# Kernel optimization log

Hardware: AMD Instinct MI355X
Metric: run time of the kernel (lower is better)

The kernel has to match this reference:

```python
import jax, jax.numpy as jnp
import numpy as np

T, B, IN, H, OUT = 2048, 64, 32, 512, 32


def setup_inputs() -> dict:
    key = jax.random.key(0)
    ks = jax.random.split(key, 7)
    s = 1.0 / np.sqrt(H)
    return {
        "inputs": jax.random.normal(ks[0], (T, B, IN), dtype=jnp.float32),
        "h0": jnp.zeros((B, H), dtype=jnp.float32),
        "c0": jnp.zeros((B, H), dtype=jnp.float32),
        "W_ih": jax.random.uniform(ks[1], (4 * H, IN), minval=-s, maxval=s, dtype=jnp.float32),
        "W_hh": jax.random.uniform(ks[2], (4 * H, H), minval=-s, maxval=s, dtype=jnp.float32),
        "b_ih": jax.random.uniform(ks[3], (4 * H,), minval=-s, maxval=s, dtype=jnp.float32),
        "b_hh": jax.random.uniform(ks[4], (4 * H,), minval=-s, maxval=s, dtype=jnp.float32),
        "W_out": jax.random.uniform(ks[5], (OUT, H), minval=-s, maxval=s, dtype=jnp.float32),
        "b_out": jax.random.uniform(ks[6], (OUT,), minval=-s, maxval=s, dtype=jnp.float32),
    }


def reference(inputs, h0, c0, W_ih, W_hh, b_ih, b_hh, W_out, b_out):
    Hh = h0.shape[-1]
    # Precompute input projections for all timesteps: [T, B, 4H]
    x_proj = jnp.einsum('tbi,gi->tbg', inputs, W_ih) + b_ih + b_hh

    def step(carry, xp):
        h, c = carry
        gates = xp + h @ W_hh.T  # [B, 4H]
        i, f, g, o = jnp.split(gates, 4, axis=-1)  # torch LSTMCell gate order
        i = jax.nn.sigmoid(i)
        f = jax.nn.sigmoid(f)
        g = jnp.tanh(g)
        o = jax.nn.sigmoid(o)
        c_new = f * c + i * g
        h_new = o * jnp.tanh(c_new)
        return (h_new, c_new), h_new

    (h_T, c_T), h_all = jax.lax.scan(step, (h0, c0), x_proj)
    outputs = jnp.einsum('tbh,oh->tbo', h_all, W_out) + b_out  # [T, B, OUT]
    return outputs, (h_T, c_T)
```

## Files before the change

kernel.cpp:

```cpp
#include <hip/hip_runtime.h>

#define TT 2048
#define BB 64
#define INF 32
#define HH 512
#define OO 32

typedef __attribute__((ext_vector_type(8))) short bf16x8;
typedef __attribute__((ext_vector_type(4))) float f32x4;

__device__ __forceinline__ float sigm(float x) {
  return 1.f / (1.f + __expf(-x));
}
__device__ __forceinline__ float tanh_(float x) {
  float e = __expf(2.f * x);
  return 1.f - 2.f / (1.f + e);
}
__device__ __forceinline__ unsigned short f2bf(float f) {
  unsigned u = __float_as_uint(f);
  u = (u + 0x7FFFu + ((u >> 16) & 1u)) >> 16;
  return (unsigned short)u;
}
__device__ __forceinline__ float bf2f(unsigned short s) {
  return __uint_as_float(((unsigned)s) << 16);
}

#define COH_LOAD4(dst, ptr)                                                  \
  asm volatile("global_load_dwordx4 %0, %1, off sc0 sc1"                     \
               : "=v"(dst) : "v"(ptr))

#define SPIN_LIMIT 20000

#define HSTR 528

__global__ __launch_bounds__(512, 2)
void lstm_fused(const float* __restrict__ X,
                const float* __restrict__ h0,
                const float* __restrict__ c0,
                const float* __restrict__ Wih,
                const float* __restrict__ Whh,
                const float* __restrict__ bih,
                const float* __restrict__ bhh,
                const float* __restrict__ Wout,
                const float* __restrict__ bout,
                float* __restrict__ outp,
                float* __restrict__ hT,
                float* __restrict__ cT,
                unsigned short* __restrict__ hring,
                int* __restrict__ flags)
{
  const int tid    = threadIdx.x;
  const int rg     = tid >> 6;
  const int lane   = tid & 63;
  const int bg     = blockIdx.x & 7;
  const int sl     = blockIdx.x >> 3;
  const int bglob0 = bg << 3;

  __shared__ __align__(16) unsigned short hlds[8 * HSTR];

  const bool mwave = (rg < 4);

  bf16x8 aW[16], aX;
  float biasf[4];
  if (mwave) {
    const int ri = lane & 15;
    const int arow = ((ri & 3) << 9) + (sl << 4) + (rg << 2) + (ri >> 2);
    const float* wb = Whh + (size_t)arow * HH + ((lane >> 4) << 3);
#pragma unroll
    for (int kt = 0; kt < 16; ++kt) {
      float4 a = ((const float4*)(wb + kt * 32))[0];
      float4 b = ((const float4*)(wb + kt * 32))[1];
      bf16x8 f;
      f[0] = (short)f2bf(a.x); f[1] = (short)f2bf(a.y);
      f[2] = (short)f2bf(a.z); f[3] = (short)f2bf(a.w);
      f[4] = (short)f2bf(b.x); f[5] = (short)f2bf(b.y);
      f[6] = (short)f2bf(b.z); f[7] = (short)f2bf(b.w);
      aW[kt] = f;
    }
    const float* wi = Wih + (size_t)arow * INF + ((lane >> 4) << 3);
    float4 a = ((const float4*)wi)[0];
    float4 b = ((const float4*)wi)[1];
    aX[0] = (short)f2bf(a.x); aX[1] = (short)f2bf(a.y);
    aX[2] = (short)f2bf(a.z); aX[3] = (short)f2bf(a.w);
    aX[4] = (short)f2bf(b.x); aX[5] = (short)f2bf(b.y);
    aX[6] = (short)f2bf(b.z); aX[7] = (short)f2bf(b.w);
#pragma unroll
    for (int r = 0; r < 4; ++r) {
      int grow = (r << 9) + (sl << 4) + (rg << 2) + (lane >> 4);
      biasf[r] = bih[grow] + bhh[grow];
    }
  }
  float wout[8];
  {
    const float4* wp = (const float4*)(Wout + sl * HH + (lane << 3));
    float4 a = wp[0], b4 = wp[1];
    wout[0] = a.x;  wout[1] = a.y;  wout[2] = a.z;  wout[3] = a.w;
    wout[4] = b4.x; wout[5] = b4.y; wout[6] = b4.z; wout[7] = b4.w;
  }
  const float bo = bout[sl];

  const bool owner = mwave && ((lane & 15) < 8);
  const int ob = lane & 7;
  const int ojj = (rg << 2) + (lane >> 4);
  const int hoff_owner = (bglob0 + ob) * HH + (sl << 4) + ojj;
  float cst = owner ? c0[hoff_owner] : 0.f;

  const int lb = tid >> 6, lg = tid & 63;
  int* myflags = flags + (bg << 5);

  for (int t = 0; t < TT; ++t) {
    bf16x8 bx;
    if (mwave) {
      const float* xr = X + (size_t)t * BB * INF + (bglob0 + (lane & 7)) * INF
                        + ((lane >> 4) << 3);
      float4 xva = ((const float4*)xr)[0];
      float4 xvb = ((const float4*)xr)[1];
      bx[0] = (short)f2bf(xva.x); bx[1] = (short)f2bf(xva.y);
      bx[2] = (short)f2bf(xva.z); bx[3] = (short)f2bf(xva.w);
      bx[4] = (short)f2bf(xvb.x); bx[5] = (short)f2bf(xvb.y);
      bx[6] = (short)f2bf(xvb.z); bx[7] = (short)f2bf(xvb.w);
    }

    if (t > 0) {
      int f = __hip_atomic_load(&myflags[lane & 31], __ATOMIC_RELAXED,
                                __HIP_MEMORY_SCOPE_AGENT);
      int guard = 0;
      while (__any(f < t)) {
        if (++guard > SPIN_LIMIT) break;
        __builtin_amdgcn_s_sleep(1);
        f = __hip_atomic_load(&myflags[lane & 31], __ATOMIC_RELAXED,
                              __HIP_MEMORY_SCOPE_AGENT);
      }
    }

    if (t == 0) {
      const float* hp = h0 + (size_t)(bglob0 + lb) * HH + (lg << 3);
      float4 a = ((const float4*)hp)[0];
      float4 b = ((const float4*)hp)[1];
      unsigned d0 = (unsigned)f2bf(a.x) | ((unsigned)f2bf(a.y) << 16);
      unsigned d1 = (unsigned)f2bf(a.z) | ((unsigned)f2bf(a.w) << 16);
      unsigned d2 = (unsigned)f2bf(b.x) | ((unsigned)f2bf(b.y) << 16);
      unsigned d3 = (unsigned)f2bf(b.z) | ((unsigned)f2bf(b.w) << 16);
      *(int4*)(hlds + lb * HSTR + (lg << 3)) = make_int4(d0, d1, d2, d3);
    } else {
      const unsigned short* hsrc = hring + (size_t)((t - 1) & 1) * BB * HH
                                   + (size_t)(bglob0 + lb) * HH + (lg << 3);
      int4 hv;
      COH_LOAD4(hv, hsrc);
      asm volatile("s_waitcnt vmcnt(0)" ::: "memory");
      __builtin_amdgcn_sched_barrier(0);
      *(int4*)(hlds + lb * HSTR + (lg << 3)) = hv;
    }
    __syncthreads();

    float o0 = 0.f, o1 = 0.f;
    if (mwave) {
      f32x4 acc0 = {0.f, 0.f, 0.f, 0.f};
      f32x4 acc1 = {0.f, 0.f, 0.f, 0.f};
      acc0 = __builtin_amdgcn_mfma_f32_16x16x32_bf16(aX, bx, acc0, 0, 0, 0);
      const unsigned short* hb = hlds + (lane & 7) * HSTR + ((lane >> 4) << 3);
#pragma unroll
      for (int kt = 0; kt < 16; kt += 2) {
        bf16x8 bf0 = *(const bf16x8*)(hb + kt * 32);
        bf16x8 bf1 = *(const bf16x8*)(hb + (kt + 1) * 32);
        acc0 = __builtin_amdgcn_mfma_f32_16x16x32_bf16(aW[kt], bf0, acc0, 0, 0, 0);
        acc1 = __builtin_amdgcn_mfma_f32_16x16x32_bf16(aW[kt + 1], bf1, acc1, 0, 0, 0);
      }
      float i_ = sigm(acc0[0] + acc1[0] + biasf[0]);
      float f_ = sigm(acc0[1] + acc1[1] + biasf[1]);
      float g_ = tanh_(acc0[2] + acc1[2] + biasf[2]);
      float o_ = sigm(acc0[3] + acc1[3] + biasf[3]);
      float cnew = __fmaf_rn(f_, cst, i_ * g_);
      float hv = o_ * tanh_(cnew);
      if (owner) cst = cnew;
      float hv2 = __shfl(hv, (lane + 16) & 63, 64);
      if (owner && ((lane >> 4) & 1) == 0) {
        unsigned pk = (unsigned)f2bf(hv) | ((unsigned)f2bf(hv2) << 16);
        unsigned* slot32 = (unsigned*)(hring + (size_t)(t & 1) * BB * HH);
        __hip_atomic_store(
            &slot32[((bglob0 + ob) << 8) + (sl << 3) + (rg << 1) + (lane >> 5)],
            pk, __ATOMIC_RELAXED, __HIP_MEMORY_SCOPE_AGENT);
      }
      if (owner && t == TT - 1) { hT[hoff_owner] = hv; cT[hoff_owner] = cst; }
    } else {
      const int wb2 = (rg - 4) << 1;
      const bf16x8 ha = *(const bf16x8*)(hlds + wb2 * HSTR + (lane << 3));
      const bf16x8 hc = *(const bf16x8*)(hlds + (wb2 + 1) * HSTR + (lane << 3));
#pragma unroll
      for (int j = 0; j < 8; ++j) {
        o0 = __fmaf_rn(bf2f((unsigned short)ha[j]), wout[j], o0);
        o1 = __fmaf_rn(bf2f((unsigned short)hc[j]), wout[j], o1);
      }
#pragma unroll
      for (int s = 32; s >= 1; s >>= 1) {
        o0 += __shfl_xor(o0, s, 64);
        o1 += __shfl_xor(o1, s, 64);
      }
    }
    __syncthreads();
    if (tid == 0)
      __hip_atomic_store(&myflags[sl], t + 1, __ATOMIC_RELAXED,
                         __HIP_MEMORY_SCOPE_AGENT);
    if (!mwave && t > 0 && lane == 0) {
      const int wb2 = (rg - 4) << 1;
      outp[(size_t)(t - 1) * BB * OO + (bglob0 + wb2) * OO + sl] = o0 + bo;
      outp[(size_t)(t - 1) * BB * OO + (bglob0 + wb2 + 1) * OO + sl] = o1 + bo;
    }
  }

  {
    int f = __hip_atomic_load(&myflags[lane & 31], __ATOMIC_RELAXED,
                              __HIP_MEMORY_SCOPE_AGENT);
    int guard = 0;
    while (__any(f < TT)) {
      if (++guard > SPIN_LIMIT) break;
      __builtin_amdgcn_s_sleep(1);
      f = __hip_atomic_load(&myflags[lane & 31], __ATOMIC_RELAXED,
                            __HIP_MEMORY_SCOPE_AGENT);
    }
  }
  {
    const unsigned short* hb = hring + (size_t)((TT - 1) & 1) * BB * HH
                               + (size_t)(bglob0 + rg) * HH + (lane << 3);
    int4 p;
    COH_LOAD4(p, hb);
    asm volatile("s_waitcnt vmcnt(0)" ::: "memory");
    __builtin_amdgcn_sched_barrier(0);
    float oacc =
        __uint_as_float(((unsigned)p.x) << 16)        * wout[0] +
        __uint_as_float(((unsigned)p.x) & 0xFFFF0000u) * wout[1] +
        __uint_as_float(((unsigned)p.y) << 16)        * wout[2] +
        __uint_as_float(((unsigned)p.y) & 0xFFFF0000u) * wout[3] +
        __uint_as_float(((unsigned)p.z) << 16)        * wout[4] +
        __uint_as_float(((unsigned)p.z) & 0xFFFF0000u) * wout[5] +
        __uint_as_float(((unsigned)p.w) << 16)        * wout[6] +
        __uint_as_float(((unsigned)p.w) & 0xFFFF0000u) * wout[7];
#pragma unroll
    for (int s = 32; s >= 1; s >>= 1) oacc += __shfl_xor(oacc, s, 64);
    if (lane == 0)
      outp[(size_t)(TT - 1) * BB * OO + (bglob0 + rg) * OO + sl] = oacc + bo;
  }
}

extern "C" void kernel_launch(void* const* d_in, const int* in_sizes, int n_in,
                              void* d_out, int out_size, void* d_ws, size_t ws_size,
                              hipStream_t stream) {
  const float* X    = (const float*)d_in[0];
  const float* h0   = (const float*)d_in[1];
  const float* c0   = (const float*)d_in[2];
  const float* Wih  = (const float*)d_in[3];
  const float* Whh  = (const float*)d_in[4];
  const float* bih  = (const float*)d_in[5];
  const float* bhh  = (const float*)d_in[6];
  const float* Wout = (const float*)d_in[7];
  const float* bout = (const float*)d_in[8];

  float* outp = (float*)d_out;
  float* hT   = outp + (size_t)TT * BB * OO;
  float* cT   = hT + (size_t)BB * HH;

  unsigned short* hring = (unsigned short*)d_ws;
  int* flags = (int*)((char*)d_ws + (size_t)2 * BB * HH * sizeof(unsigned short));

  hipMemsetAsync(flags, 0, 8 * 32 * sizeof(int), stream);

  lstm_fused<<<dim3(256), dim3(512), 0, stream>>>(
      X, h0, c0, Wih, Whh, bih, bhh, Wout, bout, outp, hT, cT, hring, flags);
}
```

Before: 3.961 ms.

## Replace flag-based inter-block sync with parity-tagged bf16 data polling

Removes the per-step flag stores, the flag spin-wait and the second __syncthreads. Consumers now poll the h ring buffer directly, using the low mantissa bit of each bf16 value as a timestep parity tag. A three-slot ring and a double-buffered LDS copy let blocks move ahead without overwriting data still being read. Forcing the parity bit costs one bit of bf16 precision, and the lowered spin limit weakens the safety fallback if a producer stalls.

Result: slower. 9.212 ms (+132.5%).

```diff
diff --git a/kernel.cpp b/kernel.cpp
--- a/kernel.cpp
+++ b/kernel.cpp
@@ -24,12 +24,19 @@
 __device__ __forceinline__ float bf2f(unsigned short s) {
   return __uint_as_float(((unsigned)s) << 16);
 }
+__device__ __forceinline__ unsigned short f2bf_par(float f, unsigned par) {
+  unsigned x = __float_as_uint(f);
+  unsigned cand = ((x >> 17) << 1) | par;
+  int diff = (int)(x - (cand << 16));
+  if (diff > 0x10000) cand += 2;
+  return (unsigned short)cand;
+}
 
 #define COH_LOAD4(dst, ptr)                                                  \
   asm volatile("global_load_dwordx4 %0, %1, off sc0 sc1"                     \
                : "=v"(dst) : "v"(ptr))
 
-#define SPIN_LIMIT 20000
+#define SPIN_LIMIT 3000
 
 #define HSTR 528
 
@@ -46,8 +53,7 @@
                 float* __restrict__ outp,
                 float* __restrict__ hT,
                 float* __restrict__ cT,
-                unsigned short* __restrict__ hring,
-                int* __restrict__ flags)
+                unsigned short* __restrict__ hring)
 {
   const int tid    = threadIdx.x;
   const int rg     = tid >> 6;
@@ -56,7 +62,7 @@
   const int sl     = blockIdx.x >> 3;
   const int bglob0 = bg << 3;
 
-  __shared__ __align__(16) unsigned short hlds[8 * HSTR];
+  __shared__ __align__(16) unsigned short hlds[2][8 * HSTR];
 
   const bool mwave = (rg < 4);
 
@@ -106,9 +112,12 @@
   float cst = owner ? c0[hoff_owner] : 0.f;
 
   const int lb = tid >> 6, lg = tid & 63;
-  int* myflags = flags + (bg << 5);
+
+  int rslot = 2, wslot = 0;
 
   for (int t = 0; t < TT; ++t) {
+    const int rbuf = t & 1;
+
     bf16x8 bx;
     if (mwave) {
       const float* xr = X + (size_t)t * BB * INF + (bglob0 + (lane & 7)) * INF
@@ -121,18 +130,6 @@
       bx[6] = (short)f2bf(xvb.z); bx[7] = (short)f2bf(xvb.w);
     }
 
-    if (t > 0) {
-      int f = __hip_atomic_load(&myflags[lane & 31], __ATOMIC_RELAXED,
-                                __HIP_MEMORY_SCOPE_AGENT);
-      int guard = 0;
-      while (__any(f < t)) {
-        if (++guard > SPIN_LIMIT) break;
-        __builtin_amdgcn_s_sleep(1);
-        f = __hip_atomic_load(&myflags[lane & 31], __ATOMIC_RELAXED,
-                              __HIP_MEMORY_SCOPE_AGENT);
-      }
-    }
-
     if (t == 0) {
       const float* hp = h0 + (size_t)(bglob0 + lb) * HH + (lg << 3);
       float4 a = ((const float4*)hp)[0];
@@ -141,24 +138,32 @@
       unsigned d1 = (unsigned)f2bf(a.z) | ((unsigned)f2bf(a.w) << 16);
       unsigned d2 = (unsigned)f2bf(b.x) | ((unsigned)f2bf(b.y) << 16);
       unsigned d3 = (unsigned)f2bf(b.z) | ((unsigned)f2bf(b.w) << 16);
-      *(int4*)(hlds + lb * HSTR + (lg << 3)) = make_int4(d0, d1, d2, d3);
+      *(int4*)(&hlds[rbuf][lb * HSTR + (lg << 3)]) = make_int4(d0, d1, d2, d3);
     } else {
-      const unsigned short* hsrc = hring + (size_t)((t - 1) & 1) * BB * HH
-                                   + (size_t)(bglob0 + lb) * HH + (lg << 3);
+      const unsigned short* src = hring + (size_t)rslot * BB * HH
+                                  + (size_t)(bglob0 + lb) * HH + (lg << 3);
+      const unsigned pp = ((t - 1) & 1) ? 0x00010001u : 0u;
       int4 hv;
-      COH_LOAD4(hv, hsrc);
-      asm volatile("s_waitcnt vmcnt(0)" ::: "memory");
-      __builtin_amdgcn_sched_barrier(0);
-      *(int4*)(hlds + lb * HSTR + (lg << 3)) = hv;
+      int guard = 0;
+      for (;;) {
+        COH_LOAD4(hv, src);
+        asm volatile("s_waitcnt vmcnt(0)" ::: "memory");
+        __builtin_amdgcn_sched_barrier(0);
+        bool ok = ((((unsigned)hv.x ^ pp) & 0x00010001u) == 0u) &
+                  ((((unsigned)hv.y ^ pp) & 0x00010001u) == 0u) &
+                  ((((unsigned)hv.z ^ pp) & 0x00010001u) == 0u) &
+                  ((((unsigned)hv.w ^ pp) & 0x00010001u) == 0u);
+        if (__all(ok) || ++guard > SPIN_LIMIT) break;
+      }
+      *(int4*)(&hlds[rbuf][lb * HSTR + (lg << 3)]) = hv;
     }
     __syncthreads();
 
-    float o0 = 0.f, o1 = 0.f;
     if (mwave) {
       f32x4 acc0 = {0.f, 0.f, 0.f, 0.f};
       f32x4 acc1 = {0.f, 0.f, 0.f, 0.f};
       acc0 = __builtin_amdgcn_mfma_f32_16x16x32_bf16(aX, bx, acc0, 0, 0, 0);
-      const unsigned short* hb = hlds + (lane & 7) * HSTR + ((lane >> 4) << 3);
+      const unsigned short* hb = &hlds[rbuf][(lane & 7) * HSTR + ((lane >> 4) << 3)];
 #pragma unroll
       for (int kt = 0; kt < 16; kt += 2) {
         bf16x8 bf0 = *(const bf16x8*)(hb + kt * 32);
@@ -175,8 +180,10 @@
       if (owner) cst = cnew;
       float hv2 = __shfl(hv, (lane + 16) & 63, 64);
       if (owner && ((lane >> 4) & 1) == 0) {
-        unsigned pk = (unsigned)f2bf(hv) | ((unsigned)f2bf(hv2) << 16);
-        unsigned* slot32 = (unsigned*)(hring + (size_t)(t & 1) * BB * HH);
+        const unsigned par = (unsigned)(t & 1);
+        unsigned pk = (unsigned)f2bf_par(hv, par)
+                    | ((unsigned)f2bf_par(hv2, par) << 16);
+        unsigned* slot32 = (unsigned*)(hring + (size_t)wslot * BB * HH);
         __hip_atomic_store(
             &slot32[((bglob0 + ob) << 8) + (sl << 3) + (rg << 1) + (lane >> 5)],
             pk, __ATOMIC_RELAXED, __HIP_MEMORY_SCOPE_AGENT);
@@ -184,8 +191,9 @@
       if (owner && t == TT - 1) { hT[hoff_owner] = hv; cT[hoff_owner] = cst; }
     } else {
       const int wb2 = (rg - 4) << 1;
-      const bf16x8 ha = *(const bf16x8*)(hlds + wb2 * HSTR + (lane << 3));
-      const bf16x8 hc = *(const bf16x8*)(hlds + (wb2 + 1) * HSTR + (lane << 3));
+      const bf16x8 ha = *(const bf16x8*)(&hlds[rbuf][wb2 * HSTR + (lane << 3)]);
+      const bf16x8 hc = *(const bf16x8*)(&hlds[rbuf][(wb2 + 1) * HSTR + (lane << 3)]);
+      float o0 = 0.f, o1 = 0.f;
 #pragma unroll
       for (int j = 0; j < 8; ++j) {
         o0 = __fmaf_rn(bf2f((unsigned short)ha[j]), wout[j], o0);
@@ -196,44 +204,39 @@
         o0 += __shfl_xor(o0, s, 64);
         o1 += __shfl_xor(o1, s, 64);
       }
-    }
-    __syncthreads();
-    if (tid == 0)
-      __hip_atomic_store(&myflags[sl], t + 1, __ATOMIC_RELAXED,
-                         __HIP_MEMORY_SCOPE_AGENT);
-    if (!mwave && t > 0 && lane == 0) {
-      const int wb2 = (rg - 4) << 1;
-      outp[(size_t)(t - 1) * BB * OO + (bglob0 + wb2) * OO + sl] = o0 + bo;
-      outp[(size_t)(t - 1) * BB * OO + (bglob0 + wb2 + 1) * OO + sl] = o1 + bo;
-    }
+      if (t > 0 && lane == 0) {
+        outp[(size_t)(t - 1) * BB * OO + (bglob0 + wb2) * OO + sl] = o0 + bo;
+        outp[(size_t)(t - 1) * BB * OO + (bglob0 + wb2 + 1) * OO + sl] = o1 + bo;
+      }
+    }
+    rslot = wslot;
+    wslot = (wslot == 2) ? 0 : wslot + 1;
   }
 
   {
-    int f = __hip_atomic_load(&myflags[lane & 31], __ATOMIC_RELAXED,
-                              __HIP_MEMORY_SCOPE_AGENT);
+    const unsigned short* src = hring + (size_t)rslot * BB * HH
+                                + (size_t)(bglob0 + rg) * HH + (lane << 3);
+    const unsigned pp = ((TT - 1) & 1) ? 0x00010001u : 0u;
+    int4 p;
     int guard = 0;
-    while (__any(f < TT)) {
-      if (++guard > SPIN_LIMIT) break;
-      __builtin_amdgcn_s_sleep(1);
-      f = __hip_atomic_load(&myflags[lane & 31], __ATOMIC_RELAXED,
-                            __HIP_MEMORY_SCOPE_AGENT);
-    }
-  }
-  {
-    const unsigned short* hb = hring + (size_t)((TT - 1) & 1) * BB * HH
-                               + (size_t)(bglob0 + rg) * HH + (lane << 3);
-    int4 p;
-    COH_LOAD4(p, hb);
-    asm volatile("s_waitcnt vmcnt(0)" ::: "memory");
-    __builtin_amdgcn_sched_barrier(0);
+    for (;;) {
+      COH_LOAD4(p, src);
+      asm volatile("s_waitcnt vmcnt(0)" ::: "memory");
+      __builtin_amdgcn_sched_barrier(0);
+      bool ok = ((((unsigned)p.x ^ pp) & 0x00010001u) == 0u) &
+                ((((unsigned)p.y ^ pp) & 0x00010001u) == 0u) &
+                ((((unsigned)p.z ^ pp) & 0x00010001u) == 0u) &
+                ((((unsigned)p.w ^ pp) & 0x00010001u) == 0u);
+      if (__all(ok) || ++guard > SPIN_LIMIT) break;
+    }
     float oacc =
-        __uint_as_float(((unsigned)p.x) << 16)        * wout[0] +
+        __uint_as_float(((unsigned)p.x) << 16)         * wout[0] +
         __uint_as_float(((unsigned)p.x) & 0xFFFF0000u) * wout[1] +
-        __uint_as_float(((unsigned)p.y) << 16)        * wout[2] +
+        __uint_as_float(((unsigned)p.y) << 16)         * wout[2] +
         __uint_as_float(((unsigned)p.y) & 0xFFFF0000u) * wout[3] +
-        __uint_as_float(((unsigned)p.z) << 16)        * wout[4] +
+        __uint_as_float(((unsigned)p.z) << 16)         * wout[4] +
         __uint_as_float(((unsigned)p.z) & 0xFFFF0000u) * wout[5] +
-        __uint_as_float(((unsigned)p.w) << 16)        * wout[6] +
+        __uint_as_float(((unsigned)p.w) << 16)         * wout[6] +
         __uint_as_float(((unsigned)p.w) & 0xFFFF0000u) * wout[7];
 #pragma unroll
     for (int s = 32; s >= 1; s >>= 1) oacc += __shfl_xor(oacc, s, 64);
@@ -260,10 +263,12 @@
   float* cT   = hT + (size_t)BB * HH;
 
   unsigned short* hring = (unsigned short*)d_ws;
-  int* flags = (int*)((char*)d_ws + (size_t)2 * BB * HH * sizeof(unsigned short));
-
-  hipMemsetAsync(flags, 0, 8 * 32 * sizeof(int), stream);
+
+  const size_t slotB = (size_t)BB * HH * sizeof(unsigned short);
+  hipMemsetAsync((char*)d_ws + 0 * slotB, 0x01, slotB, stream);
+  hipMemsetAsync((char*)d_ws + 1 * slotB, 0x00, slotB, stream);
+  hipMemsetAsync((char*)d_ws + 2 * slotB, 0x01, slotB, stream);
 
   lstm_fused<<<dim3(256), dim3(512), 0, stream>>>(
-      X, h0, c0, Wih, Whh, bih, bhh, Wout, bout, outp, hT, cT, hring, flags);
-}
+      X, h0, c0, Wih, Whh, bih, bhh, Wout, bout, outp, hT, cT, hring);
+}
```
